# Performance work log

Measured on AMD Instinct MI355X. Metric: run time of the kernel, lower is better.

Reference implementation:

```python
import jax, jax.numpy as jnp
import numpy as np

KLD_BINS = 10
RATIO_KLD = 0.5
# categorical one-hot blocks in the 99-dim Adult encoding
BLOCKS = [(1, 8), (8, 24), (24, 31), (31, 45), (45, 51), (51, 53), (53, 55), (58, 99)]
CONT_COLS = np.array([0, 55, 56, 57])


def _cross_entropy(logits, onehot):
    # F.cross_entropy with targets = argmax of the one-hot block (mean over batch)
    logp = jax.nn.log_softmax(logits, axis=-1)
    return -jnp.mean(jnp.sum(onehot * logp, axis=-1))


def _kl_divergence(p, q):
    # np-style KL: sum p*log(p/q) over valid (nonzero) bins
    valid = (p > 0) & (q > 0)
    ratio = jnp.where(valid, p / jnp.where(valid, q, 1.0), 1.0)
    return jnp.sum(jnp.where(valid, p * jnp.log(ratio), 0.0))


def setup_inputs() -> dict:
    B = 262144
    key = jax.random.key(0)
    ks = jax.random.split(key, 16)
    data_decoded = jax.random.normal(ks[0], (B, 99), dtype=jnp.float32)
    # data_true: continuous columns + one-hot categorical blocks
    data_true = jnp.zeros((B, 99), dtype=jnp.float32)
    data_true = data_true.at[:, CONT_COLS].set(jax.random.normal(ks[1], (B, 4), dtype=jnp.float32))
    for j, (s, e) in enumerate(BLOCKS):
        lab = jax.random.randint(ks[2 + j], (B,), 0, e - s)
        data_true = data_true.at[:, s:e].set(jax.nn.one_hot(lab, e - s, dtype=jnp.float32))
    data_encoded = jax.random.normal(ks[11], (B, 12), dtype=jnp.float32)
    sex = jax.random.bernoulli(ks[12], 0.5, (B,)).astype(jnp.float32)
    data_encoded = data_encoded.at[:, 11].set(sex)  # column 11 of combined is the 0/1 sex neuron
    label_true = jax.random.normal(ks[13], (B, 2), dtype=jnp.float32)
    return {
        'data_encoded': data_encoded,
        'data_decoded': data_decoded,
        'data_true': data_true,
        'label_true': label_true,
        'batch_size': B,
    }


def reference(data_encoded, data_decoded, data_true, label_true, batch_size):
    # --- reconstruction MSE on continuous columns ---
    cc = jnp.asarray(CONT_COLS)
    mse_loss = jnp.sum(jnp.mean((data_decoded[:, cc] - data_true[:, cc]) ** 2, axis=0))
    # --- cross-entropy on each categorical block ---
    ce_loss = jnp.float32(0.0)
    for s, e in BLOCKS:
        ce_loss = ce_loss + _cross_entropy(data_decoded[:, s:e], data_true[:, s:e])
    # --- per-feature histogram KLD between male/female groups (no grad, as in torch via .numpy()) ---
    comb = jnp.concatenate([data_encoded, label_true], axis=1)  # [B, 14]
    feats = comb[:, :KLD_BINS]  # first 10 encoded features, [B, 10]
    mn = jnp.min(feats, axis=0)  # per-column min over full batch (torch .item())
    mx = jnp.max(feats, axis=0)
    width = jnp.maximum(mx - mn, 1e-12)
    # torch.histc bin index: floor((x-min)/(max-min)*bins), x==max -> last bin
    idx = jnp.clip(jnp.floor((feats - mn) / width * KLD_BINS).astype(jnp.int32), 0, KLD_BINS - 1)
    onehot = jax.nn.one_hot(idx, KLD_BINS, dtype=jnp.float32)  # [B, 10, bins]
    sexcol = comb[:, 11]
    m_mask = (sexcol == 0).astype(jnp.float32)
    f_mask = (sexcol == 1).astype(jnp.float32)
    m_count = jnp.maximum(jnp.sum(m_mask), 1.0)
    f_count = jnp.maximum(jnp.sum(f_mask), 1.0)
    m_hist = jnp.einsum('b,bik->ik', m_mask, onehot) / m_count  # [10, bins]
    f_hist = jnp.einsum('b,bik->ik', f_mask, onehot) / f_count
    kld = jax.lax.stop_gradient(_kl_divergence(m_hist, f_hist))
    alpha = RATIO_KLD
    multi_loss = (1.0 - alpha) * (mse_loss + ce_loss) + alpha * kld
    return (multi_loss, mse_loss, ce_loss, alpha * kld)
```

## Files before the change

kernel.cpp:

```cpp
#include <hip/hip_runtime.h>
#include <math.h>

#define B_ROWS 262144

#define WS_A 0
#define WS_B 2816
#define WS_C 28416
#define MAIN_BLOCKS 768
#define N_STREAMS (MAIN_BLOCKS * 4)
#define TILE_ROWS 8
#define N_TILES 32768
#define TILE_F4 198

__device__ __forceinline__ unsigned int map_f(float x) {
  unsigned int b = __float_as_uint(x);
  return (b & 0x80000000u) ? ~b : (b | 0x80000000u);
}
__device__ __forceinline__ float unmap_f(unsigned int u) {
  unsigned int b = (u & 0x80000000u) ? (u ^ 0x80000000u) : ~u;
  return __uint_as_float(b);
}

__global__ __launch_bounds__(256) void k_minmax(const float* __restrict__ enc,
                                                unsigned int* __restrict__ ws) {
  int tid = threadIdx.x, bid = blockIdx.x;
  const float4* e4 = (const float4*)enc;
  float mn[10], mx[10];
  #pragma unroll
  for (int j = 0; j < 10; j++) { mn[j] = 1e30f; mx[j] = -1e30f; }
  unsigned int cm = 0, cf = 0;
  #pragma unroll
  for (int i = 0; i < 8; i++) {
    size_t g = (size_t)bid * 2048 + i * 256 + tid;
    float4 a = e4[g * 3 + 0], b = e4[g * 3 + 1], c = e4[g * 3 + 2];
    float v[12] = {a.x,a.y,a.z,a.w,b.x,b.y,b.z,b.w,c.x,c.y,c.z,c.w};
    #pragma unroll
    for (int j = 0; j < 10; j++) { mn[j] = fminf(mn[j], v[j]); mx[j] = fmaxf(mx[j], v[j]); }
    cm += (v[11] == 0.0f); cf += (v[11] == 1.0f);
  }
  #pragma unroll
  for (int off = 32; off; off >>= 1) {
    #pragma unroll
    for (int j = 0; j < 10; j++) {
      mn[j] = fminf(mn[j], __shfl_xor(mn[j], off));
      mx[j] = fmaxf(mx[j], __shfl_xor(mx[j], off));
    }
    cm += __shfl_xor(cm, off); cf += __shfl_xor(cf, off);
  }
  __shared__ float smn[4][10], smx[4][10];
  __shared__ unsigned int sc[4][2];
  int wave = tid >> 6, lane = tid & 63;
  if (lane == 0) {
    #pragma unroll
    for (int j = 0; j < 10; j++) { smn[wave][j] = mn[j]; smx[wave][j] = mx[j]; }
    sc[wave][0] = cm; sc[wave][1] = cf;
  }
  __syncthreads();
  unsigned int* out = ws + WS_A + bid * 22;
  if (tid < 10) {
    float m = fminf(fminf(smn[0][tid], smn[1][tid]), fminf(smn[2][tid], smn[3][tid]));
    out[tid] = map_f(m);
  } else if (tid < 20) {
    int j = tid - 10;
    float m = fmaxf(fmaxf(smx[0][j], smx[1][j]), fmaxf(smx[2][j], smx[3][j]));
    out[tid] = map_f(m);
  } else if (tid < 22) {
    int j = tid - 20;
    out[tid] = sc[0][j] + sc[1][j] + sc[2][j] + sc[3][j];
  }
}

__global__ __launch_bounds__(256) void k_hist(const float* __restrict__ enc,
                                              unsigned int* __restrict__ ws) {
  __shared__ float mnv[10], wid[10];
  __shared__ unsigned int h[200];
  int tid = threadIdx.x, bid = blockIdx.x;
  for (int i = tid; i < 200; i += 256) h[i] = 0u;
  if (tid < 10) {
    unsigned int umn = 0xFFFFFFFFu, umx = 0u;
    #pragma unroll 4
    for (int b = 0; b < 128; b++) {
      umn = min(umn, ws[WS_A + b * 22 + tid]);
      umx = max(umx, ws[WS_A + b * 22 + 10 + tid]);
    }
    float mn = unmap_f(umn);
    mnv[tid] = mn;
    wid[tid] = fmaxf(unmap_f(umx) - mn, 1e-12f);
  }
  __syncthreads();
  const float4* e4 = (const float4*)enc;
  #pragma unroll
  for (int i = 0; i < 8; i++) {
    size_t g = (size_t)bid * 2048 + i * 256 + tid;
    float4 a = e4[g * 3 + 0], b = e4[g * 3 + 1], c = e4[g * 3 + 2];
    float v[12] = {a.x,a.y,a.z,a.w,b.x,b.y,b.z,b.w,c.x,c.y,c.z,c.w};
    int base = (v[11] == 0.0f) ? 0 : ((v[11] == 1.0f) ? 100 : -1);
    if (base >= 0) {
      #pragma unroll
      for (int cc = 0; cc < 10; cc++) {
        float t = (v[cc] - mnv[cc]) / wid[cc] * 10.0f;
        int bi = min(max((int)floorf(t), 0), 9);
        atomicAdd(&h[base + cc * 10 + bi], 1u);
      }
    }
  }
  __syncthreads();
  if (tid < 200) ws[WS_B + bid * 200 + tid] = h[tid];
}

__device__ __forceinline__ void issue_tile(const float* __restrict__ d,
                                           const float* __restrict__ t,
                                           int tile, int lane,
                                           float* bd, float* bt) {
  const float4* dsp = (const float4*)d + (size_t)tile * TILE_F4;
  const float4* tsp = (const float4*)t + (size_t)tile * TILE_F4;
  #pragma unroll
  for (int it = 0; it < 3; ++it) {
    __builtin_amdgcn_global_load_lds(
        (const __attribute__((address_space(1))) void*)(dsp + it * 64 + lane),
        (__attribute__((address_space(3))) void*)(bd + it * 256), 16, 0, 0);
    __builtin_amdgcn_global_load_lds(
        (const __attribute__((address_space(1))) void*)(tsp + it * 64 + lane),
        (__attribute__((address_space(3))) void*)(bt + it * 256), 16, 0, 0);
  }
  if (lane < 6) {
    __builtin_amdgcn_global_load_lds(
        (const __attribute__((address_space(1))) void*)(dsp + 192 + lane),
        (__attribute__((address_space(3))) void*)(bd + 768), 16, 0, 0);
    __builtin_amdgcn_global_load_lds(
        (const __attribute__((address_space(1))) void*)(tsp + 192 + lane),
        (__attribute__((address_space(3))) void*)(bt + 768), 16, 0, 0);
  }
}

__device__ __forceinline__ void compute_tile(const float* bd, const float* bt,
                                             int lane,
                                             float& mse, float& dot, float& ce) {
  const float4* ld4 = (const float4*)bd;
  const float4* lt4 = (const float4*)bt;
  #pragma unroll
  for (int it = 0; it < 4; ++it) {
    int f = it * 64 + lane;
    if (f < TILE_F4) {
      float4 xd = ld4[f];
      float4 xt = lt4[f];
      int e = f * 4;
      int c = e - (e / 99) * 99;
      float dv[4] = {xd.x, xd.y, xd.z, xd.w};
      float tw[4] = {xt.x, xt.y, xt.z, xt.w};
      #pragma unroll
      for (int k = 0; k < 4; k++) {
        int cc = c + k;
        if (cc >= 99) cc -= 99;
        bool cont = (cc == 0) | ((unsigned)(cc - 55) <= 2u);
        float diff = dv[k] - tw[k];
        if (cont) mse += diff * diff;
        else      dot += tw[k] * dv[k];
      }
    }
  }
  if (lane < 2 * TILE_ROWS) {
    const float* row = bd + (lane >> 1) * 99;
    float Z;
    if ((lane & 1) == 0) {
      Z = 0.f;
      #pragma unroll
      for (int c = 1; c < 8; c++) Z += __expf(row[c]);
      ce += __logf(Z);
      Z = 0.f;
      #pragma unroll
      for (int c = 8; c < 24; c++) Z += __expf(row[c]);
      ce += __logf(Z);
      Z = 0.f;
      #pragma unroll
      for (int c = 24; c < 31; c++) Z += __expf(row[c]);
      ce += __logf(Z);
      Z = 0.f;
      #pragma unroll
      for (int c = 31; c < 45; c++) Z += __expf(row[c]);
      ce += __logf(Z);
      Z = 0.f;
      #pragma unroll
      for (int c = 45; c < 51; c++) Z += __expf(row[c]);
      ce += __logf(Z);
    } else {
      Z = 0.f;
      #pragma unroll
      for (int c = 51; c < 53; c++) Z += __expf(row[c]);
      ce += __logf(Z);
      Z = 0.f;
      #pragma unroll
      for (int c = 53; c < 55; c++) Z += __expf(row[c]);
      ce += __logf(Z);
      Z = 0.f;
      #pragma unroll
      for (int c = 58; c < 99; c++) Z += __expf(row[c]);
      ce += __logf(Z);
    }
  }
}

__global__ __launch_bounds__(256, 3) void k_main(const float* __restrict__ d,
                                                 const float* __restrict__ t,
                                                 unsigned int* __restrict__ ws) {
  __shared__ float sd[4][2][2][800];
  __shared__ float red[12];
  int tid = threadIdx.x, bid = blockIdx.x;
  int wave = tid >> 6, lane = tid & 63;
  float* base = &sd[wave][0][0][0];

  float mse = 0.f, dot = 0.f, ce = 0.f;
  int gw = bid * 4 + wave;

  int p = 0;
  int tile = gw;
  issue_tile(d, t, tile, lane, base, base + 800);
  while (tile + N_STREAMS < N_TILES) {
    int nx = tile + N_STREAMS;
    float* nb = base + (p ^ 1) * 1600;
    issue_tile(d, t, nx, lane, nb, nb + 800);
    asm volatile("s_waitcnt vmcnt(8)" ::: "memory");
    __builtin_amdgcn_sched_barrier(0);
    float* cb = base + p * 1600;
    compute_tile(cb, cb + 800, lane, mse, dot, ce);
    p ^= 1;
    tile = nx;
  }
  asm volatile("s_waitcnt vmcnt(0)" ::: "memory");
  __builtin_amdgcn_sched_barrier(0);
  {
    float* cb = base + p * 1600;
    compute_tile(cb, cb + 800, lane, mse, dot, ce);
  }

  #pragma unroll
  for (int off = 32; off; off >>= 1) {
    mse += __shfl_xor(mse, off);
    dot += __shfl_xor(dot, off);
    ce  += __shfl_xor(ce,  off);
  }
  if (lane == 0) { red[wave] = mse; red[4 + wave] = dot; red[8 + wave] = ce; }
  __syncthreads();
  if (tid == 0) {
    float* C = (float*)(ws + WS_C);
    C[bid]                   = red[0] + red[1] + red[2]  + red[3];
    C[MAIN_BLOCKS + bid]     = red[4] + red[5] + red[6]  + red[7];
    C[2 * MAIN_BLOCKS + bid] = red[8] + red[9] + red[10] + red[11];
  }
}

__global__ __launch_bounds__(256) void k_final(const unsigned int* __restrict__ ws,
                                               float* __restrict__ out) {
  __shared__ float h[200];
  __shared__ float part[256];
  __shared__ float red3[12];
  __shared__ float cnts[2];
  int tid = threadIdx.x;
  if (tid < 200) {
    unsigned int s = 0;
    #pragma unroll 4
    for (int b = 0; b < 128; b++) s += ws[WS_B + b * 200 + tid];
    h[tid] = (float)s;
  }
  if (tid == 200 || tid == 201) {
    unsigned int s = 0;
    #pragma unroll 4
    for (int b = 0; b < 128; b++) s += ws[WS_A + b * 22 + 20 + (tid - 200)];
    cnts[tid - 200] = fmaxf((float)s, 1.0f);
  }
  const float* C = (const float*)(ws + WS_C);
  float msum = 0.f, dsum = 0.f, csum = 0.f;
  for (int i = tid; i < MAIN_BLOCKS; i += 256) {
    msum += C[i]; dsum += C[MAIN_BLOCKS + i]; csum += C[2 * MAIN_BLOCKS + i];
  }
  #pragma unroll
  for (int off = 32; off; off >>= 1) {
    msum += __shfl_xor(msum, off);
    dsum += __shfl_xor(dsum, off);
    csum += __shfl_xor(csum, off);
  }
  int wave = tid >> 6, lane = tid & 63;
  if (lane == 0) { red3[wave] = msum; red3[4 + wave] = dsum; red3[8 + wave] = csum; }
  __syncthreads();
  float term = 0.f;
  if (tid < 100) {
    float mc = h[tid], fc = h[100 + tid];
    if (mc > 0.f && fc > 0.f) {
      float p = mc / cnts[0];
      float q = fc / cnts[1];
      term = p * logf(p / q);
    }
  }
  part[tid] = term;
  __syncthreads();
  for (int s = 128; s; s >>= 1) {
    if (tid < s) part[tid] += part[tid + s];
    __syncthreads();
  }
  if (tid == 0) {
    const float invB = 1.0f / (float)B_ROWS;
    float mse = (red3[0] + red3[1] + red3[2] + red3[3]) * invB;
    float dd  = (red3[4] + red3[5] + red3[6] + red3[7]);
    float cc  = (red3[8] + red3[9] + red3[10] + red3[11]);
    float ce  = (cc - dd) * invB;
    float akld = 0.5f * part[0];
    out[0] = 0.5f * (mse + ce) + akld;
    out[1] = mse;
    out[2] = ce;
    out[3] = akld;
  }
}

extern "C" void kernel_launch(void* const* d_in, const int* in_sizes, int n_in,
                              void* d_out, int out_size, void* d_ws, size_t ws_size,
                              hipStream_t stream) {
  const float* enc = (const float*)d_in[0];
  const float* dec = (const float*)d_in[1];
  const float* tru = (const float*)d_in[2];
  unsigned int* ws = (unsigned int*)d_ws;
  float* out = (float*)d_out;

  hipLaunchKernelGGL(k_minmax, dim3(128),         dim3(256), 0, stream, enc, ws);
  hipLaunchKernelGGL(k_hist,   dim3(128),         dim3(256), 0, stream, enc, ws);
  hipLaunchKernelGGL(k_main,   dim3(MAIN_BLOCKS), dim3(256), 0, stream, dec, tru, ws);
  hipLaunchKernelGGL(k_final,  dim3(1),           dim3(256), 0, stream, ws, out);
}
```

Measured before the change: 290.3 us.

## Stream targets via registers, precompute exp in LDS, double occupancy, atomic histogram merge

Targets are now loaded straight into registers instead of through LDS, which halves LDS use per wave and allows six blocks per CU with twice as many main blocks. The sweep pass computes exp once per element and writes it back to LDS, so the per-row log-sum-exp becomes a plain sum. Per-block histograms are merged with global atomics into one slot, zeroed by the minmax kernel, so the final kernel no longer loops over 128 copies. The risks are more register pressure from the target loads and hand-written waitcnt counts that must match the new load pattern.

```diff
diff --git a/kernel.cpp b/kernel.cpp
--- a/kernel.cpp
+++ b/kernel.cpp
@@ -5,8 +5,8 @@
 
 #define WS_A 0
 #define WS_B 2816
-#define WS_C 28416
-#define MAIN_BLOCKS 768
+#define WS_C 3072
+#define MAIN_BLOCKS 1536
 #define N_STREAMS (MAIN_BLOCKS * 4)
 #define TILE_ROWS 8
 #define N_TILES 32768
@@ -67,6 +67,9 @@
   } else if (tid < 22) {
     int j = tid - 20;
     out[tid] = sc[0][j] + sc[1][j] + sc[2][j] + sc[3][j];
+  }
+  if (bid == 0) {
+    for (int i = tid; i < 200; i += 256) ws[WS_B + i] = 0u;
   }
 }
 
@@ -105,45 +108,44 @@
     }
   }
   __syncthreads();
-  if (tid < 200) ws[WS_B + bid * 200 + tid] = h[tid];
-}
-
-__device__ __forceinline__ void issue_tile(const float* __restrict__ d,
-                                           const float* __restrict__ t,
-                                           int tile, int lane,
-                                           float* bd, float* bt) {
+  if (tid < 200) atomicAdd(ws + WS_B + tid, h[tid]);
+}
+
+__device__ __forceinline__ void issue_d(const float* __restrict__ d,
+                                        int tile, int lane, float* bd) {
   const float4* dsp = (const float4*)d + (size_t)tile * TILE_F4;
-  const float4* tsp = (const float4*)t + (size_t)tile * TILE_F4;
-  #pragma unroll
-  for (int it = 0; it < 3; ++it) {
+  #pragma unroll
+  for (int it = 0; it < 3; ++it)
     __builtin_amdgcn_global_load_lds(
         (const __attribute__((address_space(1))) void*)(dsp + it * 64 + lane),
         (__attribute__((address_space(3))) void*)(bd + it * 256), 16, 0, 0);
-    __builtin_amdgcn_global_load_lds(
-        (const __attribute__((address_space(1))) void*)(tsp + it * 64 + lane),
-        (__attribute__((address_space(3))) void*)(bt + it * 256), 16, 0, 0);
-  }
-  if (lane < 6) {
+  if (lane < 6)
     __builtin_amdgcn_global_load_lds(
         (const __attribute__((address_space(1))) void*)(dsp + 192 + lane),
         (__attribute__((address_space(3))) void*)(bd + 768), 16, 0, 0);
-    __builtin_amdgcn_global_load_lds(
-        (const __attribute__((address_space(1))) void*)(tsp + 192 + lane),
-        (__attribute__((address_space(3))) void*)(bt + 768), 16, 0, 0);
-  }
-}
-
-__device__ __forceinline__ void compute_tile(const float* bd, const float* bt,
-                                             int lane,
-                                             float& mse, float& dot, float& ce) {
-  const float4* ld4 = (const float4*)bd;
-  const float4* lt4 = (const float4*)bt;
+}
+
+__device__ __forceinline__ void load_t(const float* __restrict__ t, int tile,
+                                       int lane, float4& r0, float4& r1,
+                                       float4& r2, float4& r3) {
+  const float4* tsp = (const float4*)t + (size_t)tile * TILE_F4;
+  r0 = tsp[lane];
+  r1 = tsp[64 + lane];
+  r2 = tsp[128 + lane];
+  r3 = tsp[192 + ((lane < 6) ? lane : 0)];
+}
+
+__device__ __forceinline__ void sweep_tile(float* bd, float4 t0, float4 t1,
+                                           float4 t2, float4 t3, int lane,
+                                           float& mse, float& dot) {
+  float4* b4 = (float4*)bd;
+  float4 tvv[4] = {t0, t1, t2, t3};
   #pragma unroll
   for (int it = 0; it < 4; ++it) {
     int f = it * 64 + lane;
-    if (f < TILE_F4) {
-      float4 xd = ld4[f];
-      float4 xt = lt4[f];
+    if (it < 3 || lane < 6) {
+      float4 xd = b4[f];
+      float4 xt = tvv[it];
       int e = f * 4;
       int c = e - (e / 99) * 99;
       float dv[4] = {xd.x, xd.y, xd.z, xd.w};
@@ -157,80 +159,94 @@
         if (cont) mse += diff * diff;
         else      dot += tw[k] * dv[k];
       }
-    }
-  }
+      float4 ev;
+      ev.x = __expf(xd.x); ev.y = __expf(xd.y);
+      ev.z = __expf(xd.z); ev.w = __expf(xd.w);
+      b4[f] = ev;
+    }
+  }
+}
+
+__device__ __forceinline__ void lse_adds(const float* bd, int lane, float& ce) {
   if (lane < 2 * TILE_ROWS) {
     const float* row = bd + (lane >> 1) * 99;
     float Z;
     if ((lane & 1) == 0) {
       Z = 0.f;
       #pragma unroll
-      for (int c = 1; c < 8; c++) Z += __expf(row[c]);
-      ce += __logf(Z);
-      Z = 0.f;
-      #pragma unroll
-      for (int c = 8; c < 24; c++) Z += __expf(row[c]);
-      ce += __logf(Z);
-      Z = 0.f;
-      #pragma unroll
-      for (int c = 24; c < 31; c++) Z += __expf(row[c]);
-      ce += __logf(Z);
-      Z = 0.f;
-      #pragma unroll
-      for (int c = 31; c < 45; c++) Z += __expf(row[c]);
-      ce += __logf(Z);
-      Z = 0.f;
-      #pragma unroll
-      for (int c = 45; c < 51; c++) Z += __expf(row[c]);
+      for (int c = 1; c < 8; c++) Z += row[c];
+      ce += __logf(Z);
+      Z = 0.f;
+      #pragma unroll
+      for (int c = 8; c < 24; c++) Z += row[c];
+      ce += __logf(Z);
+      Z = 0.f;
+      #pragma unroll
+      for (int c = 24; c < 31; c++) Z += row[c];
+      ce += __logf(Z);
+      Z = 0.f;
+      #pragma unroll
+      for (int c = 31; c < 45; c++) Z += row[c];
+      ce += __logf(Z);
+      Z = 0.f;
+      #pragma unroll
+      for (int c = 45; c < 51; c++) Z += row[c];
       ce += __logf(Z);
     } else {
       Z = 0.f;
       #pragma unroll
-      for (int c = 51; c < 53; c++) Z += __expf(row[c]);
-      ce += __logf(Z);
-      Z = 0.f;
-      #pragma unroll
-      for (int c = 53; c < 55; c++) Z += __expf(row[c]);
-      ce += __logf(Z);
-      Z = 0.f;
-      #pragma unroll
-      for (int c = 58; c < 99; c++) Z += __expf(row[c]);
-      ce += __logf(Z);
-    }
-  }
-}
-
-__global__ __launch_bounds__(256, 3) void k_main(const float* __restrict__ d,
+      for (int c = 51; c < 53; c++) Z += row[c];
+      ce += __logf(Z);
+      Z = 0.f;
+      #pragma unroll
+      for (int c = 53; c < 55; c++) Z += row[c];
+      ce += __logf(Z);
+      float Za = 0.f, Zb = 0.f;
+      #pragma unroll
+      for (int c = 58; c < 78; c++) Za += row[c];
+      #pragma unroll
+      for (int c = 78; c < 99; c++) Zb += row[c];
+      ce += __logf(Za + Zb);
+    }
+  }
+}
+
+__global__ __launch_bounds__(256, 6) void k_main(const float* __restrict__ d,
                                                  const float* __restrict__ t,
                                                  unsigned int* __restrict__ ws) {
-  __shared__ float sd[4][2][2][800];
+  __shared__ float sd[4][2][800];
   __shared__ float red[12];
   int tid = threadIdx.x, bid = blockIdx.x;
   int wave = tid >> 6, lane = tid & 63;
-  float* base = &sd[wave][0][0][0];
+  float* base = &sd[wave][0][0];
 
   float mse = 0.f, dot = 0.f, ce = 0.f;
   int gw = bid * 4 + wave;
 
   int p = 0;
   int tile = gw;
-  issue_tile(d, t, tile, lane, base, base + 800);
-  while (tile + N_STREAMS < N_TILES) {
+  issue_d(d, tile, lane, base);
+  float4 t0, t1, t2, t3;
+  load_t(t, tile, lane, t0, t1, t2, t3);
+  for (;;) {
     int nx = tile + N_STREAMS;
-    float* nb = base + (p ^ 1) * 1600;
-    issue_tile(d, t, nx, lane, nb, nb + 800);
-    asm volatile("s_waitcnt vmcnt(8)" ::: "memory");
+    bool hn = nx < N_TILES;
+    if (hn) {
+      issue_d(d, nx, lane, base + (p ^ 1) * 800);
+      asm volatile("s_waitcnt vmcnt(8)" ::: "memory");
+    } else {
+      asm volatile("s_waitcnt vmcnt(4)" ::: "memory");
+    }
     __builtin_amdgcn_sched_barrier(0);
-    float* cb = base + p * 1600;
-    compute_tile(cb, cb + 800, lane, mse, dot, ce);
+    float* cb = base + p * 800;
+    sweep_tile(cb, t0, t1, t2, t3, lane, mse, dot);
+    if (hn) load_t(t, nx, lane, t0, t1, t2, t3);
+    asm volatile("s_waitcnt lgkmcnt(0)" ::: "memory");
+    __builtin_amdgcn_sched_barrier(0);
+    lse_adds(cb, lane, ce);
+    if (!hn) break;
     p ^= 1;
     tile = nx;
-  }
-  asm volatile("s_waitcnt vmcnt(0)" ::: "memory");
-  __builtin_amdgcn_sched_barrier(0);
-  {
-    float* cb = base + p * 1600;
-    compute_tile(cb, cb + 800, lane, mse, dot, ce);
   }
 
   #pragma unroll
@@ -256,12 +272,7 @@
   __shared__ float red3[12];
   __shared__ float cnts[2];
   int tid = threadIdx.x;
-  if (tid < 200) {
-    unsigned int s = 0;
-    #pragma unroll 4
-    for (int b = 0; b < 128; b++) s += ws[WS_B + b * 200 + tid];
-    h[tid] = (float)s;
-  }
+  if (tid < 200) h[tid] = (float)ws[WS_B + tid];
   if (tid == 200 || tid == 201) {
     unsigned int s = 0;
     #pragma unroll 4
```

Result: faster. 277.8 us (-4.3%).
